# Kernel optimization log

Hardware: AMD Instinct MI355X
Metric: run time of the kernel (lower is better)

The kernel has to match this reference:

```python
import jax, jax.numpy as jnp
import numpy as np

B, N, H, NH = 8, 1024, 512, 8
DK = H // NH


def setup_inputs() -> dict:
    key = jax.random.key(0)
    ks = jax.random.split(key, 6)
    x = jax.random.normal(ks[0], (B, N, H), dtype=jnp.float32)
    adj = jax.random.randint(ks[1], (B, N, N), 0, 2, dtype=jnp.int32)
    # ensure no all-zero row (self-loops) so softmax is well-defined
    adj = jnp.maximum(adj, jnp.eye(N, dtype=jnp.int32)[None])
    s = 1.0 / np.sqrt(H)
    Wq = jax.random.normal(ks[2], (H, H), dtype=jnp.float32) * s
    Wk = jax.random.normal(ks[3], (H, H), dtype=jnp.float32) * s
    Wv = jax.random.normal(ks[4], (H, H), dtype=jnp.float32) * s
    Wg = jax.random.normal(ks[5], (H, 2 * H), dtype=jnp.float32) * (1.0 / np.sqrt(2 * H))
    bg = jnp.zeros((H,), dtype=jnp.float32)
    return {"x": x, "adj": adj, "Wq": Wq, "Wk": Wk, "Wv": Wv, "Wg": Wg, "bg": bg}


def reference(x, adj, Wq, Wk, Wv, Wg, bg):
    b, n, h = x.shape
    # projections (nn.Linear: x @ W.T), split heads -> [b, n, nh, dk]
    q = (x @ Wq.T).reshape(b, n, NH, DK)
    k = (x @ Wk.T).reshape(b, n, NH, DK)
    v = (x @ Wv.T).reshape(b, n, NH, DK)
    # scaled masked attention: [b, nh, n, n]
    scores = jnp.einsum('bqhd,bkhd->bhqk', q, k) / jnp.sqrt(jnp.float32(DK))
    mask = (adj != 0)[:, None, :, :]
    scores = jnp.where(mask, scores, -jnp.inf)
    attn = jax.nn.softmax(scores, axis=-1)  # dropout p=0.0 -> identity
    c = jnp.einsum('bhqk,bkhd->bqhd', attn, v).reshape(b, n, h)
    # sigmoid gated residual combine
    gate = jax.nn.sigmoid(jnp.concatenate([c, x], axis=2) @ Wg.T + bg)
    return gate * x + (1.0 - gate) * c
```

## Files before the change

kernel.cpp:

```cpp
#include <hip/hip_runtime.h>
#include <math.h>

#define B_  8
#define N_  1024
#define H_  512
#define NH_ 8
#define DK_ 64
#define M_  (B_ * N_)

typedef __attribute__((ext_vector_type(4))) float f32x4;
typedef __attribute__((ext_vector_type(8))) short bf16x8;

__device__ __forceinline__ unsigned short f2bf(float f) {
    unsigned int u = __float_as_uint(f);
    u = (u + 0x7fffu + ((u >> 16) & 1u)) >> 16;
    return (unsigned short)u;
}

__device__ __forceinline__ float fexp2(float x) {
#if __has_builtin(__builtin_amdgcn_exp2f)
    return __builtin_amdgcn_exp2f(x);
#else
    return exp2f(x);
#endif
}

__device__ __forceinline__ void gload16(const unsigned short* g, unsigned short* l) {
    __builtin_amdgcn_global_load_lds(
        (const __attribute__((address_space(1))) void*)g,
        (__attribute__((address_space(3))) void*)l, 16, 0, 0);
}

__global__ __launch_bounds__(256) void cvt_all_k(const float* __restrict__ x,
                                                 const float* __restrict__ Wq,
                                                 const float* __restrict__ Wk,
                                                 const float* __restrict__ Wv,
                                                 const float* __restrict__ Wg,
                                                 unsigned short* __restrict__ xb,
                                                 unsigned short* __restrict__ wqb,
                                                 unsigned short* __restrict__ wkb,
                                                 unsigned short* __restrict__ wvb,
                                                 unsigned short* __restrict__ wgb)
{
    int id = blockIdx.x;
    const float* src; unsigned short* dst; int off; float scale = 1.0f;
    if (id < 4096)      { src = x;  dst = xb;  off = id; }
    else if (id < 4352) { src = Wq; dst = wqb; off = id - 4096; scale = 0.18033688011112042f; }
    else if (id < 4608) { src = Wk; dst = wkb; off = id - 4352; }
    else if (id < 4864) { src = Wv; dst = wvb; off = id - 4608; }
    else                { src = Wg; dst = wgb; off = id - 4864; }
    size_t i = (size_t)off * 1024 + threadIdx.x * 4;
    float4 v = *(const float4*)&src[i];
    *(ushort4*)&dst[i] = make_ushort4(f2bf(v.x * scale), f2bf(v.y * scale),
                                      f2bf(v.z * scale), f2bf(v.w * scale));
}

__global__ __launch_bounds__(256) void pack_k(const int* __restrict__ adj,
                                              unsigned long long* __restrict__ mb)
{
    int gw   = (int)((blockIdx.x * 256 + threadIdx.x) >> 6);
    int lane = threadIdx.x & 63;
    int kt = gw & 15;
    int q  = (gw >> 4) & (N_ - 1);
    int b  = gw >> 14;
    int val = adj[(size_t)(b * N_ + q) * N_ + kt * 64 + lane];
    unsigned long long m = __ballot(val != 0);
    if (lane == 0) mb[gw] = m;
}

__global__ __launch_bounds__(256, 3) void proj_k(const unsigned short* __restrict__ xb,
                                                 const unsigned short* __restrict__ Wqb,
                                                 const unsigned short* __restrict__ Wkb,
                                                 const unsigned short* __restrict__ Wvb,
                                                 unsigned short* __restrict__ qkv)
{
    __shared__ unsigned short As[8192];
    __shared__ unsigned short Bs[8192];
    const int tid = threadIdx.x;
    const int lane = tid & 63, wv = tid >> 6;
    const int ln = lane & 15, quad = lane >> 4;
    const int wm = wv >> 1, wn = wv & 1;
    const int row0 = blockIdx.x * 128;
    const int w    = blockIdx.y >> 2;
    const int col0 = (blockIdx.y & 3) * 128;
    const unsigned short* W = (w == 0) ? Wqb : ((w == 1) ? Wkb : Wvb);
    f32x4 acc[4][4] = {};

    for (int kt = 0; kt < H_; kt += 64) {
        __syncthreads();
        #pragma unroll
        for (int i = 0; i < 4; ++i) {
            int c = tid + i * 256;
            int c8 = c >> 7, row = c & 127;
            gload16(&xb[(size_t)(row0 + row) * H_ + kt + c8 * 8], &As[c * 8]);
            gload16(&W [(size_t)(col0 + row) * H_ + kt + c8 * 8], &Bs[c * 8]);
        }
        __syncthreads();
        #pragma unroll
        for (int kk = 0; kk < 2; ++kk) {
            bf16x8 af[4], bf[4];
            #pragma unroll
            for (int t = 0; t < 4; ++t) {
                af[t] = *(const bf16x8*)&As[((kk * 4 + quad) * 128 + wm * 64 + t * 16 + ln) * 8];
                bf[t] = *(const bf16x8*)&Bs[((kk * 4 + quad) * 128 + wn * 64 + t * 16 + ln) * 8];
            }
            #pragma unroll
            for (int mt = 0; mt < 4; ++mt)
                #pragma unroll
                for (int nt = 0; nt < 4; ++nt)
                    acc[mt][nt] = __builtin_amdgcn_mfma_f32_16x16x32_bf16(af[mt], bf[nt], acc[mt][nt], 0, 0, 0);
        }
    }
    #pragma unroll
    for (int mt = 0; mt < 4; ++mt)
        #pragma unroll
        for (int nt = 0; nt < 4; ++nt)
            #pragma unroll
            for (int r = 0; r < 4; ++r) {
                int m = row0 + wm * 64 + mt * 16 + quad * 4 + r;
                int c = w * H_ + col0 + wn * 64 + nt * 16 + ln;
                qkv[(size_t)m * (3 * H_) + c] = f2bf(acc[mt][nt][r]);
            }
}

__global__ __launch_bounds__(256) void transp_k(const unsigned short* __restrict__ qkv,
                                                unsigned short* __restrict__ Vt)
{
    __shared__ unsigned short Ts[64][72];
    const int bh = blockIdx.x;
    const int n0 = blockIdx.y * 64;
    const int b = bh >> 3, h = bh & 7;
    const int tid = threadIdx.x;
    #pragma unroll
    for (int p = 0; p < 2; ++p) {
        int row = (tid >> 3) + p * 32;
        int ch  = tid & 7;
        *(uint4*)&Ts[row][ch * 8] =
            *(const uint4*)&qkv[(size_t)(b * N_ + n0 + row) * (3 * H_) + 2 * H_ + h * DK_ + ch * 8];
    }
    __syncthreads();
    #pragma unroll
    for (int p = 0; p < 16; ++p) {
        int d = (tid >> 6) + p * 4;
        int n = tid & 63;
        Vt[((size_t)bh * DK_ + d) * N_ + n0 + n] = Ts[n][d];
    }
}

__global__ __launch_bounds__(256, 2) void attn_k(const unsigned short* __restrict__ qkv,
                                                 const unsigned short* __restrict__ Vt,
                                                 const unsigned long long* __restrict__ Mb,
                                                 unsigned short* __restrict__ Cmb)
{
    const int nqt  = N_ / 128;
    const int qt   = blockIdx.x % nqt;
    const int head = (blockIdx.x / nqt) % NH_;
    const int b    = blockIdx.x / (nqt * NH_);

    __shared__ unsigned short Ks[2][4096];
    __shared__ unsigned short Vs[2][4096];
    __shared__ unsigned short Ps[4][2][16][72];

    const int tid = threadIdx.x;
    const int lane = tid & 63, wv = tid >> 6;
    const int ln = lane & 15, quad = lane >> 4;
    const int q0 = qt * 128 + wv * 32 + ln;
    const int q1 = q0 + 16;

    const unsigned short* Kbase = qkv + H_ + head * DK_;
    const unsigned short* Vbase = Vt + (size_t)(b * NH_ + head) * DK_ * N_;

    bf16x8 bq[2][2];
    #pragma unroll
    for (int kk = 0; kk < 2; ++kk) {
        bq[0][kk] = *(const bf16x8*)&qkv[(size_t)(b * N_ + q0) * (3 * H_) + head * DK_ + kk * 32 + quad * 8];
        bq[1][kk] = *(const bf16x8*)&qkv[(size_t)(b * N_ + q1) * (3 * H_) + head * DK_ + kk * 32 + quad * 8];
    }

    f32x4 o[2][4] = {};
    float psum[2] = {0.f, 0.f};

    auto issue = [&](int t, int bi) {
        #pragma unroll
        for (int i = 0; i < 2; ++i) {
            int c = tid + i * 256;
            int c8 = c >> 6, row = c & 63;
            gload16(&Kbase[(size_t)(b * N_ + t * 64 + row) * (3 * H_) + c8 * 8], &Ks[bi][c * 8]);
            gload16(&Vbase[(size_t)row * N_ + t * 64 + c8 * 8], &Vs[bi][c * 8]);
        }
    };

    issue(0, 0);

    for (int t = 0; t < 16; ++t) {
        __syncthreads();
        if (t < 15) issue(t + 1, (t + 1) & 1);
        const unsigned short* Kc = Ks[t & 1];
        const unsigned short* Vc = Vs[t & 1];

        unsigned long long mq[2];
        mq[0] = Mb[(size_t)(b * N_ + q0) * 16 + t];
        mq[1] = Mb[(size_t)(b * N_ + q1) * 16 + t];

        f32x4 s[2][4] = {};
        #pragma unroll
        for (int kk = 0; kk < 2; ++kk)
            #pragma unroll
            for (int nt = 0; nt < 4; ++nt) {
                bf16x8 ka = *(const bf16x8*)&Kc[((kk * 4 + quad) * 64 + nt * 16 + ln) * 8];
                s[0][nt] = __builtin_amdgcn_mfma_f32_16x16x32_bf16(ka, bq[0][kk], s[0][nt], 0, 0, 0);
                s[1][nt] = __builtin_amdgcn_mfma_f32_16x16x32_bf16(ka, bq[1][kk], s[1][nt], 0, 0, 0);
            }

        #pragma unroll
        for (int g = 0; g < 2; ++g) {
            unsigned long long sh = mq[g] >> (quad * 4);
            #pragma unroll
            for (int nt = 0; nt < 4; ++nt) {
                unsigned int bn = (unsigned int)(sh >> (nt * 16)) & 0xFu;
                float p[4];
                #pragma unroll
                for (int r = 0; r < 4; ++r) {
                    float e = fexp2(s[g][nt][r]);
                    p[r] = (bn & (1u << r)) ? e : 0.f;
                    psum[g] += p[r];
                }
                unsigned int d0 = __builtin_amdgcn_perm(__float_as_uint(p[1]), __float_as_uint(p[0]), 0x07060302u);
                unsigned int d1 = __builtin_amdgcn_perm(__float_as_uint(p[3]), __float_as_uint(p[2]), 0x07060302u);
                *(uint2*)&Ps[wv][g][ln][nt * 16 + quad * 4] = make_uint2(d0, d1);
            }
        }

        bf16x8 pb[2][2];
        #pragma unroll
        for (int g = 0; g < 2; ++g)
            #pragma unroll
            for (int kk = 0; kk < 2; ++kk)
                pb[g][kk] = *(const bf16x8*)&Ps[wv][g][ln][kk * 32 + quad * 8];

        #pragma unroll
        for (int kk = 0; kk < 2; ++kk)
            #pragma unroll
            for (int dt = 0; dt < 4; ++dt) {
                bf16x8 va = *(const bf16x8*)&Vc[((kk * 4 + quad) * 64 + dt * 16 + ln) * 8];
                o[0][dt] = __builtin_amdgcn_mfma_f32_16x16x32_bf16(va, pb[0][kk], o[0][dt], 0, 0, 0);
                o[1][dt] = __builtin_amdgcn_mfma_f32_16x16x32_bf16(va, pb[1][kk], o[1][dt], 0, 0, 0);
            }
    }

    #pragma unroll
    for (int g = 0; g < 2; ++g) {
        psum[g] += __shfl_xor(psum[g], 16);
        psum[g] += __shfl_xor(psum[g], 32);
        float inv = 1.f / psum[g];
        int qg = (g == 0) ? q0 : q1;
        #pragma unroll
        for (int dt = 0; dt < 4; ++dt) {
            ushort4 u = make_ushort4(f2bf(o[g][dt][0] * inv), f2bf(o[g][dt][1] * inv),
                                     f2bf(o[g][dt][2] * inv), f2bf(o[g][dt][3] * inv));
            *(ushort4*)&Cmb[(size_t)(b * N_ + qg) * H_ + head * DK_ + dt * 16 + quad * 4] = u;
        }
    }
}

__global__ __launch_bounds__(256, 2) void gate_k(const unsigned short* __restrict__ cmb,
                                                 const unsigned short* __restrict__ xb,
                                                 const unsigned short* __restrict__ Wgb,
                                                 const float* __restrict__ bgp,
                                                 const float* __restrict__ X,
                                                 float* __restrict__ out)
{
    __shared__ unsigned short As[8192];
    __shared__ unsigned short Bs[4096];
    const int tid = threadIdx.x;
    const int lane = tid & 63, wv = tid >> 6;
    const int ln = lane & 15, quad = lane >> 4;
    const int wm = wv >> 1, wn = wv & 1;
    const int row0 = blockIdx.x * 128;
    const int col0 = blockIdx.y * 64;
    f32x4 acc[4][2] = {};

    for (int kt = 0; kt < 2 * H_; kt += 64) {
        const unsigned short* Asrc = (kt < H_) ? cmb : xb;
        const int ko = kt & (H_ - 1);
        __syncthreads();
        #pragma unroll
        for (int i = 0; i < 4; ++i) {
            int c = tid + i * 256;
            int c8 = c >> 7, row = c & 127;
            gload16(&Asrc[(size_t)(row0 + row) * H_ + ko + c8 * 8], &As[c * 8]);
        }
        #pragma unroll
        for (int i = 0; i < 2; ++i) {
            int c = tid + i * 256;
            int c8 = c >> 6, row = c & 63;
            gload16(&Wgb[(size_t)(col0 + row) * (2 * H_) + kt + c8 * 8], &Bs[c * 8]);
        }
        __syncthreads();
        #pragma unroll
        for (int kk = 0; kk < 2; ++kk) {
            bf16x8 af[4], bf[2];
            #pragma unroll
            for (int t = 0; t < 4; ++t)
                af[t] = *(const bf16x8*)&As[((kk * 4 + quad) * 128 + wm * 64 + t * 16 + ln) * 8];
            #pragma unroll
            for (int t = 0; t < 2; ++t)
                bf[t] = *(const bf16x8*)&Bs[((kk * 4 + quad) * 64 + wn * 32 + t * 16 + ln) * 8];
            #pragma unroll
            for (int mt = 0; mt < 4; ++mt)
                #pragma unroll
                for (int nt = 0; nt < 2; ++nt)
                    acc[mt][nt] = __builtin_amdgcn_mfma_f32_16x16x32_bf16(af[mt], bf[nt], acc[mt][nt], 0, 0, 0);
        }
    }
    #pragma unroll
    for (int mt = 0; mt < 4; ++mt)
        #pragma unroll
        for (int nt = 0; nt < 2; ++nt)
            #pragma unroll
            for (int r = 0; r < 4; ++r) {
                int m = row0 + wm * 64 + mt * 16 + quad * 4 + r;
                int c = col0 + wn * 32 + nt * 16 + ln;
                float g  = 1.f / (1.f + __expf(-(acc[mt][nt][r] + bgp[c])));
                float xv = X[(size_t)m * H_ + c];
                float cv = __uint_as_float(((unsigned int)cmb[(size_t)m * H_ + c]) << 16);
                out[(size_t)m * H_ + c] = g * xv + (1.f - g) * cv;
            }
}

extern "C" void kernel_launch(void* const* d_in, const int* in_sizes, int n_in,
                              void* d_out, int out_size, void* d_ws, size_t ws_size,
                              hipStream_t stream)
{
    const float* x   = (const float*)d_in[0];
    const int*   adj = (const int*)  d_in[1];
    const float* Wq  = (const float*)d_in[2];
    const float* Wk  = (const float*)d_in[3];
    const float* Wv  = (const float*)d_in[4];
    const float* Wg  = (const float*)d_in[5];
    const float* bg  = (const float*)d_in[6];
    float* out = (float*)d_out;

    unsigned short* xb  = (unsigned short*)d_ws;
    unsigned short* wqb = xb  + (size_t)M_ * H_;
    unsigned short* wkb = wqb + (size_t)H_ * H_;
    unsigned short* wvb = wkb + (size_t)H_ * H_;
    unsigned short* wgb = wvb + (size_t)H_ * H_;
    unsigned short* qkv = wgb + (size_t)H_ * 2 * H_;
    unsigned short* vt  = qkv + (size_t)M_ * 3 * H_;
    unsigned short* cmb = vt  + (size_t)M_ * H_;
    unsigned long long* mb = (unsigned long long*)(cmb + (size_t)M_ * H_);

    cvt_all_k<<<5376, 256, 0, stream>>>(x, Wq, Wk, Wv, Wg, xb, wqb, wkb, wvb, wgb);

    pack_k<<<M_ * 16 / 4, 256, 0, stream>>>(adj, mb);

    proj_k<<<dim3(M_ / 128, 12), 256, 0, stream>>>(xb, wqb, wkb, wvb, qkv);

    transp_k<<<dim3(B_ * NH_, N_ / 64), 256, 0, stream>>>(qkv, vt);

    attn_k<<<B_ * NH_ * (N_ / 128), 256, 0, stream>>>(qkv, vt, mb, cmb);

    gate_k<<<dim3(M_ / 128, H_ / 64), 256, 0, stream>>>(cmb, xb, wgb, bg, x, out);
}
```

Before: 218.3 us.

## Split attention over key halves, merge prep kernels, vectorize V transpose

```diff
diff --git a/kernel.cpp b/kernel.cpp
--- a/kernel.cpp
+++ b/kernel.cpp
@@ -17,6 +17,10 @@
     return (unsigned short)u;
 }
 
+__device__ __forceinline__ float bf2f(unsigned short s) {
+    return __uint_as_float(((unsigned int)s) << 16);
+}
+
 __device__ __forceinline__ float fexp2(float x) {
 #if __has_builtin(__builtin_amdgcn_exp2f)
     return __builtin_amdgcn_exp2f(x);
@@ -31,18 +35,31 @@
         (__attribute__((address_space(3))) void*)l, 16, 0, 0);
 }
 
-__global__ __launch_bounds__(256) void cvt_all_k(const float* __restrict__ x,
-                                                 const float* __restrict__ Wq,
-                                                 const float* __restrict__ Wk,
-                                                 const float* __restrict__ Wv,
-                                                 const float* __restrict__ Wg,
-                                                 unsigned short* __restrict__ xb,
-                                                 unsigned short* __restrict__ wqb,
-                                                 unsigned short* __restrict__ wkb,
-                                                 unsigned short* __restrict__ wvb,
-                                                 unsigned short* __restrict__ wgb)
+__global__ __launch_bounds__(256) void prep_k(const float* __restrict__ x,
+                                              const float* __restrict__ Wq,
+                                              const float* __restrict__ Wk,
+                                              const float* __restrict__ Wv,
+                                              const float* __restrict__ Wg,
+                                              const int*   __restrict__ adj,
+                                              unsigned short* __restrict__ xb,
+                                              unsigned short* __restrict__ wqb,
+                                              unsigned short* __restrict__ wkb,
+                                              unsigned short* __restrict__ wvb,
+                                              unsigned short* __restrict__ wgb,
+                                              unsigned long long* __restrict__ mb)
 {
     int id = blockIdx.x;
+    if (id >= 5376) {
+        int gw   = (id - 5376) * 4 + (threadIdx.x >> 6);
+        int lane = threadIdx.x & 63;
+        int kt = gw & 15;
+        int q  = (gw >> 4) & (N_ - 1);
+        int b  = gw >> 14;
+        int val = adj[(size_t)(b * N_ + q) * N_ + kt * 64 + lane];
+        unsigned long long m = __ballot(val != 0);
+        if (lane == 0) mb[gw] = m;
+        return;
+    }
     const float* src; unsigned short* dst; int off; float scale = 1.0f;
     if (id < 4096)      { src = x;  dst = xb;  off = id; }
     else if (id < 4352) { src = Wq; dst = wqb; off = id - 4096; scale = 0.18033688011112042f; }
@@ -53,19 +70,6 @@
     float4 v = *(const float4*)&src[i];
     *(ushort4*)&dst[i] = make_ushort4(f2bf(v.x * scale), f2bf(v.y * scale),
                                       f2bf(v.z * scale), f2bf(v.w * scale));
-}
-
-__global__ __launch_bounds__(256) void pack_k(const int* __restrict__ adj,
-                                              unsigned long long* __restrict__ mb)
-{
-    int gw   = (int)((blockIdx.x * 256 + threadIdx.x) >> 6);
-    int lane = threadIdx.x & 63;
-    int kt = gw & 15;
-    int q  = (gw >> 4) & (N_ - 1);
-    int b  = gw >> 14;
-    int val = adj[(size_t)(b * N_ + q) * N_ + kt * 64 + lane];
-    unsigned long long m = __ballot(val != 0);
-    if (lane == 0) mb[gw] = m;
 }
 
 __global__ __launch_bounds__(256, 3) void proj_k(const unsigned short* __restrict__ xb,
@@ -140,22 +144,25 @@
     }
     __syncthreads();
     #pragma unroll
-    for (int p = 0; p < 16; ++p) {
-        int d = (tid >> 6) + p * 4;
-        int n = tid & 63;
-        Vt[((size_t)bh * DK_ + d) * N_ + n0 + n] = Ts[n][d];
-    }
-}
-
-__global__ __launch_bounds__(256, 2) void attn_k(const unsigned short* __restrict__ qkv,
+    for (int p = 0; p < 4; ++p) {
+        int d  = (tid >> 4) + p * 16;
+        int n4 = (tid & 15) * 4;
+        ushort4 u = make_ushort4(Ts[n4][d], Ts[n4 + 1][d], Ts[n4 + 2][d], Ts[n4 + 3][d]);
+        *(ushort4*)&Vt[((size_t)bh * DK_ + d) * N_ + n0 + n4] = u;
+    }
+}
+
+__global__ __launch_bounds__(256, 3) void attn_k(const unsigned short* __restrict__ qkv,
                                                  const unsigned short* __restrict__ Vt,
                                                  const unsigned long long* __restrict__ Mb,
-                                                 unsigned short* __restrict__ Cmb)
-{
-    const int nqt  = N_ / 128;
-    const int qt   = blockIdx.x % nqt;
-    const int head = (blockIdx.x / nqt) % NH_;
-    const int b    = blockIdx.x / (nqt * NH_);
+                                                 unsigned short* __restrict__ po,
+                                                 float* __restrict__ pl)
+{
+    const int qt   = blockIdx.x & 7;
+    const int head = (blockIdx.x >> 3) & 7;
+    const int b    = (blockIdx.x >> 6) & 7;
+    const int s    = blockIdx.x >> 9;
+    const int t0   = s * 8;
 
     __shared__ unsigned short Ks[2][4096];
     __shared__ unsigned short Vs[2][4096];
@@ -190,11 +197,11 @@
         }
     };
 
-    issue(0, 0);
-
-    for (int t = 0; t < 16; ++t) {
-        __syncthreads();
-        if (t < 15) issue(t + 1, (t + 1) & 1);
+    issue(t0, 0);
+
+    for (int t = t0; t < t0 + 8; ++t) {
+        __syncthreads();
+        if (t < t0 + 7) issue(t + 1, (t + 1) & 1);
         const unsigned short* Kc = Ks[t & 1];
         const unsigned short* Vc = Vs[t & 1];
 
@@ -202,14 +209,14 @@
         mq[0] = Mb[(size_t)(b * N_ + q0) * 16 + t];
         mq[1] = Mb[(size_t)(b * N_ + q1) * 16 + t];
 
-        f32x4 s[2][4] = {};
+        f32x4 sv[2][4] = {};
         #pragma unroll
         for (int kk = 0; kk < 2; ++kk)
             #pragma unroll
             for (int nt = 0; nt < 4; ++nt) {
                 bf16x8 ka = *(const bf16x8*)&Kc[((kk * 4 + quad) * 64 + nt * 16 + ln) * 8];
-                s[0][nt] = __builtin_amdgcn_mfma_f32_16x16x32_bf16(ka, bq[0][kk], s[0][nt], 0, 0, 0);
-                s[1][nt] = __builtin_amdgcn_mfma_f32_16x16x32_bf16(ka, bq[1][kk], s[1][nt], 0, 0, 0);
+                sv[0][nt] = __builtin_amdgcn_mfma_f32_16x16x32_bf16(ka, bq[0][kk], sv[0][nt], 0, 0, 0);
+                sv[1][nt] = __builtin_amdgcn_mfma_f32_16x16x32_bf16(ka, bq[1][kk], sv[1][nt], 0, 0, 0);
             }
 
         #pragma unroll
@@ -221,7 +228,7 @@
                 float p[4];
                 #pragma unroll
                 for (int r = 0; r < 4; ++r) {
-                    float e = fexp2(s[g][nt][r]);
+                    float e = fexp2(sv[g][nt][r]);
                     p[r] = (bn & (1u << r)) ? e : 0.f;
                     psum[g] += p[r];
                 }
@@ -248,19 +255,41 @@
             }
     }
 
+    unsigned short* pos = po + (size_t)s * M_ * H_;
+    float* pls = pl + (size_t)s * M_ * NH_;
     #pragma unroll
     for (int g = 0; g < 2; ++g) {
         psum[g] += __shfl_xor(psum[g], 16);
         psum[g] += __shfl_xor(psum[g], 32);
-        float inv = 1.f / psum[g];
         int qg = (g == 0) ? q0 : q1;
+        if (quad == 0) pls[(size_t)(b * N_ + qg) * NH_ + head] = psum[g];
         #pragma unroll
         for (int dt = 0; dt < 4; ++dt) {
-            ushort4 u = make_ushort4(f2bf(o[g][dt][0] * inv), f2bf(o[g][dt][1] * inv),
-                                     f2bf(o[g][dt][2] * inv), f2bf(o[g][dt][3] * inv));
-            *(ushort4*)&Cmb[(size_t)(b * N_ + qg) * H_ + head * DK_ + dt * 16 + quad * 4] = u;
-        }
-    }
+            ushort4 u = make_ushort4(f2bf(o[g][dt][0]), f2bf(o[g][dt][1]),
+                                     f2bf(o[g][dt][2]), f2bf(o[g][dt][3]));
+            *(ushort4*)&po[(size_t)s * M_ * H_ + (size_t)(b * N_ + qg) * H_ + head * DK_ + dt * 16 + quad * 4] = u;
+        }
+    }
+    (void)pos;
+}
+
+__global__ __launch_bounds__(256) void comb_k(const unsigned short* __restrict__ po,
+                                              const float* __restrict__ pl,
+                                              unsigned short* __restrict__ cmb)
+{
+    size_t i = ((size_t)blockIdx.x * 256 + threadIdx.x) * 4;
+    int m = (int)(i >> 9);
+    int f = (int)(i & 511);
+    int head = f >> 6;
+    ushort4 a = *(const ushort4*)&po[i];
+    ushort4 c = *(const ushort4*)&po[(size_t)M_ * H_ + i];
+    float l = pl[(size_t)m * NH_ + head] + pl[(size_t)M_ * NH_ + (size_t)m * NH_ + head];
+    float inv = 1.f / l;
+    ushort4 u = make_ushort4(f2bf((bf2f(a.x) + bf2f(c.x)) * inv),
+                             f2bf((bf2f(a.y) + bf2f(c.y)) * inv),
+                             f2bf((bf2f(a.z) + bf2f(c.z)) * inv),
+                             f2bf((bf2f(a.w) + bf2f(c.w)) * inv));
+    *(ushort4*)&cmb[i] = u;
 }
 
 __global__ __launch_bounds__(256, 2) void gate_k(const unsigned short* __restrict__ cmb,
@@ -323,7 +352,7 @@
                 int c = col0 + wn * 32 + nt * 16 + ln;
                 float g  = 1.f / (1.f + __expf(-(acc[mt][nt][r] + bgp[c])));
                 float xv = X[(size_t)m * H_ + c];
-                float cv = __uint_as_float(((unsigned int)cmb[(size_t)m * H_ + c]) << 16);
+                float cv = bf2f(cmb[(size_t)m * H_ + c]);
                 out[(size_t)m * H_ + c] = g * xv + (1.f - g) * cv;
             }
 }
@@ -349,17 +378,20 @@
     unsigned short* qkv = wgb + (size_t)H_ * 2 * H_;
     unsigned short* vt  = qkv + (size_t)M_ * 3 * H_;
     unsigned short* cmb = vt  + (size_t)M_ * H_;
-    unsigned long long* mb = (unsigned long long*)(cmb + (size_t)M_ * H_);
-
-    cvt_all_k<<<5376, 256, 0, stream>>>(x, Wq, Wk, Wv, Wg, xb, wqb, wkb, wvb, wgb);
-
-    pack_k<<<M_ * 16 / 4, 256, 0, stream>>>(adj, mb);
+    unsigned short* po  = cmb + (size_t)M_ * H_;
+    float*          pl  = (float*)(po + (size_t)2 * M_ * H_);
+    unsigned long long* mb = (unsigned long long*)(pl + (size_t)2 * M_ * NH_);
+
+    prep_k<<<5376 + 32768, 256, 0, stream>>>(x, Wq, Wk, Wv, Wg, adj,
+                                             xb, wqb, wkb, wvb, wgb, mb);
 
     proj_k<<<dim3(M_ / 128, 12), 256, 0, stream>>>(xb, wqb, wkb, wvb, qkv);
 
     transp_k<<<dim3(B_ * NH_, N_ / 64), 256, 0, stream>>>(qkv, vt);
 
-    attn_k<<<B_ * NH_ * (N_ / 128), 256, 0, stream>>>(qkv, vt, mb, cmb);
+    attn_k<<<B_ * NH_ * (N_ / 128) * 2, 256, 0, stream>>>(qkv, vt, mb, po, pl);
+
+    comb_k<<<M_ * H_ / 1024, 256, 0, stream>>>(po, pl, cmb);
 
     gate_k<<<dim3(M_ / 128, H_ / 64), 256, 0, stream>>>(cmb, xb, wgb, bg, x, out);
 }
```

After: 226.6 us. +3.8%, slower.
